# Kernel optimization log

Measured on AMD Instinct MI355X. Metric: run time of the kernel, lower is better.

Reference implementation:

```python
import jax, jax.numpy as jnp
import numpy as np


def _shift_lr(t):
    # t: [B, L, H] -> (left, right) neighbor states with zero padding
    B, L, H = t.shape
    pad = jnp.zeros((B, 1, H), dtype=t.dtype)
    left = jnp.concatenate([pad, t[:, :-1, :]], axis=1)
    right = jnp.concatenate([t[:, 1:, :], pad], axis=1)
    return left, right


def setup_inputs() -> dict:
    key = jax.random.key(0)
    ks = jax.random.split(key, 7)
    B, L, H = 32, 2048, 256
    h_t = jax.random.normal(ks[0], (B, L, H), dtype=jnp.float32)
    x = jax.random.normal(ks[1], (B, L, H), dtype=jnp.float32)
    h_slot = jax.random.normal(ks[2], (B, L, H), dtype=jnp.float32)
    h_intent = jax.random.normal(ks[3], (B, L, H), dtype=jnp.float32)
    c_t = jax.random.normal(ks[4], (B, L, H), dtype=jnp.float32)
    # gate order: [i, o, f, l, r, u]; linear in = 6H, out = H
    Ws = jax.random.normal(ks[5], (6, 6 * H, H), dtype=jnp.float32) * 0.02
    bs = jnp.zeros((6, H), dtype=jnp.float32)
    return {"h_t": h_t, "x": x, "h_slot": h_slot, "h_intent": h_intent,
            "c_t": c_t, "Ws": Ws, "bs": bs}


def reference(h_t, x, h_slot, h_intent, c_t, Ws, bs):
    h_left, h_right = _shift_lr(h_t)
    # concat order: [h_mid, h_left, h_right, x, h_slot, h_intent] -> [B,L,6H]
    cat = jnp.concatenate([h_t, h_left, h_right, x, h_slot, h_intent], axis=-1)
    # one batched GEMM for all six gates: [6, B, L, H]
    gates = jnp.einsum('blc,gch->gblh', cat, Ws) + bs[:, None, None, :]
    i_t = jax.nn.sigmoid(gates[0])
    o_t = jax.nn.sigmoid(gates[1])
    f_t = jax.nn.sigmoid(gates[2])
    l_t = jax.nn.sigmoid(gates[3])
    r_t = jax.nn.sigmoid(gates[4])
    u_t = jnp.tanh(gates[5])
    # softmax across the 4 gates (axis 0 of the stack)
    soft = jax.nn.softmax(jnp.stack([i_t, f_t, l_t, r_t], axis=0), axis=0)
    i_t, f_t, l_t, r_t = soft[0], soft[1], soft[2], soft[3]
    c_left, c_right = _shift_lr(c_t)
    c_new = f_t * c_t + l_t * c_left + r_t * c_right + i_t * u_t
    h_new = o_t * jnp.tanh(c_new)
    return (h_new, c_new)
```

## Files before the change

### kernel.cpp

```cpp
#include <hip/hip_runtime.h>

typedef __attribute__((ext_vector_type(8))) short short8;
typedef __attribute__((ext_vector_type(4))) float f32x4;

#define BB 32
#define LL 2048
#define HH 256
#define MTOT (BB*LL)
#define KK 1536
#define HSIZE (MTOT*HH)

#define SWZ4(v) (((v) & 3) ^ (((v) >> 2) & 3))

__device__ __forceinline__ unsigned short f2bf(float f){
    unsigned u = __builtin_bit_cast(unsigned, f);
    u += 0x7FFFu + ((u >> 16) & 1u);
    return (unsigned short)(u >> 16);
}
__device__ __forceinline__ unsigned pk2(float lo, float hi){
    return (unsigned)f2bf(lo) | ((unsigned)f2bf(hi) << 16);
}
__device__ __forceinline__ float sigm(float v){
    return 1.0f / (1.0f + __expf(-v));
}
__device__ __forceinline__ float ftanh(float v){
    v = fminf(fmaxf(v, -30.0f), 30.0f);
    float e = __expf(2.0f * v);
    return (e - 1.0f) / (e + 1.0f);
}
__device__ __forceinline__ void gload_lds16(const void* g, void* l){
    __builtin_amdgcn_global_load_lds(
        (const __attribute__((address_space(1))) unsigned int*)g,
        (__attribute__((address_space(3))) unsigned int*)l, 16, 0, 0);
}

__global__ __launch_bounds__(256) void prep_bt(const float* __restrict__ Ws,
                                               unsigned short* __restrict__ Bt){
    __shared__ float tile[64][65];
    int bid = blockIdx.x;
    int kb = bid % 24; int tmp = bid / 24; int hb = tmp & 3; int g = tmp >> 2;
    int t = threadIdx.x;
    const float* src = Ws + (size_t)g * (KK * HH) + (size_t)(kb * 64) * HH + hb * 64;
    #pragma unroll
    for (int it = 0; it < 16; ++it){
        int e = it * 256 + t; int kk = e >> 6, hh = e & 63;
        tile[kk][hh] = src[(size_t)kk * HH + hh];
    }
    __syncthreads();
    #pragma unroll
    for (int it = 0; it < 2; ++it){
        int jj  = t;
        int ksl = it;
        int hc  = jj >> 2, qp = jj & 3;
        int col = g * 64 + hc;
        int q   = qp ^ SWZ4(col);
        int kbase = ksl * 32 + q * 8;
        unsigned wz[4];
        #pragma unroll
        for (int p = 0; p < 4; ++p)
            wz[p] = pk2(tile[kbase + 2*p][hc], tile[kbase + 2*p + 1][hc]);
        int ksg = kb * 2 + ksl;
        size_t off = ((size_t)(hb * 48 + ksg) * 1536 + (size_t)g * 256 + jj) * 8;
        *(uint4*)&Bt[off] = *(uint4*)wz;
    }
}

__global__ __launch_bounds__(512, 2) void slstm_fused(
    const float* __restrict__ h_t, const float* __restrict__ x,
    const float* __restrict__ h_slot, const float* __restrict__ h_intent,
    const float* __restrict__ c_t, const float* __restrict__ bs,
    const unsigned short* __restrict__ Bt, float* __restrict__ out)
{
    __shared__ __align__(16) unsigned short As[2][128 * 32];
    __shared__ __align__(16) unsigned short Bs[2][384 * 32];

    const int t    = threadIdx.x;
    const int wv   = t >> 6,  ln  = t & 63;
    const int rg   = wv >> 2, ht  = wv & 3;
    const int quad = ln >> 4, l16 = ln & 15;

    const int rawb = blockIdx.x;
    const int vb   = (rawb & 7) * 256 + (rawb >> 3);
    const int h_chunk = vb & 3;
    const int m_block = vb >> 2;
    const int h0      = h_chunk * 64;

    const int  arow = t >> 2;
    const int  aq   = t & 3;
    const int  akq  = aq << 3;
    const long mg   = (long)m_block * 128 + arow;
    const int  lseq = (int)(mg & (LL - 1));
    const int  awq  = (aq ^ SWZ4(arow)) << 3;
    const int  qa   = (quad ^ SWZ4(l16)) << 3;

    const unsigned short* BtH = Bt + (size_t)h_chunk * 48 * 1536 * 8;

    f32x4 acc[4][6] = {};

    float4 av0, av1;
    auto stageA_issue = [&](int ks){
        int c  = ks >> 3;
        int kk = ((ks & 7) << 5) + akq;
        const float* src; int sh;
        switch (c){
            case 0:  src = h_t;      sh =  0; break;
            case 1:  src = h_t;      sh = -1; break;
            case 2:  src = h_t;      sh =  1; break;
            case 3:  src = x;        sh =  0; break;
            case 4:  src = h_slot;   sh =  0; break;
            default: src = h_intent; sh =  0; break;
        }
        int sl = lseq + sh;
        av0 = make_float4(0.f,0.f,0.f,0.f); av1 = av0;
        if ((unsigned)sl < (unsigned)LL){
            const float* p = src + ((mg + sh) * HH + kk);
            av0 = *(const float4*)p;
            av1 = *(const float4*)(p + 4);
        }
    };
    auto stageB = [&](int buf, int ks){
        const unsigned short* gsrc = BtH + (size_t)ks * 1536 * 8;
        #pragma unroll
        for (int i = 0; i < 3; ++i){
            gload_lds16(gsrc + (size_t)(i * 512 + t) * 8,
                        &Bs[buf][(i * 512 + wv * 64) * 8]);
        }
    };
    auto stageA_write = [&](int buf){
        uint4 w;
        w.x = pk2(av0.x, av0.y); w.y = pk2(av0.z, av0.w);
        w.z = pk2(av1.x, av1.y); w.w = pk2(av1.z, av1.w);
        *(uint4*)&As[buf][arow * 32 + awq] = w;
    };

    stageA_issue(0);
    stageB(0, 0);
    stageA_write(0);
    __syncthreads();

    for (int ks = 0; ks < 48; ++ks){
        const int cur = ks & 1, nxt = cur ^ 1;
        if (ks < 47){
            stageA_issue(ks + 1);
            stageB(nxt, ks + 1);
        }
        short8 a[4];
        #pragma unroll
        for (int mt = 0; mt < 4; ++mt)
            a[mt] = *(const short8*)&As[cur][(rg * 64 + mt * 16 + l16) * 32 + qa];
        #pragma unroll
        for (int g = 0; g < 6; ++g){
            short8 bfrag = *(const short8*)&Bs[cur][(g * 64 + ht * 16 + l16) * 32 + qa];
            #pragma unroll
            for (int mt = 0; mt < 4; ++mt)
                acc[mt][g] = __builtin_amdgcn_mfma_f32_16x16x32_bf16(a[mt], bfrag, acc[mt][g], 0, 0, 0);
        }
        if (ks < 47) stageA_write(nxt);
        __syncthreads();
    }

    const int h = h0 + ht * 16 + l16;
    float bias[6];
    #pragma unroll
    for (int g = 0; g < 6; ++g) bias[g] = bs[g * HH + h];

    #pragma unroll
    for (int mt = 0; mt < 4; ++mt){
        #pragma unroll
        for (int r = 0; r < 4; ++r){
            long row = (long)m_block * 128 + rg * 64 + mt * 16 + quad * 4 + r;
            int  ls  = (int)(row & (LL - 1));
            float gi = sigm(acc[mt][0][r] + bias[0]);
            float go = sigm(acc[mt][1][r] + bias[1]);
            float gf = sigm(acc[mt][2][r] + bias[2]);
            float gl = sigm(acc[mt][3][r] + bias[3]);
            float gr = sigm(acc[mt][4][r] + bias[4]);
            float gu = ftanh(acc[mt][5][r] + bias[5]);
            float ei = __expf(gi), ef = __expf(gf), el = __expf(gl), er = __expf(gr);
            float inv = 1.0f / (ei + ef + el + er);
            float cm  = c_t[row * HH + h];
            float clv = (ls > 0)      ? c_t[(row - 1) * HH + h] : 0.0f;
            float crv = (ls < LL - 1) ? c_t[(row + 1) * HH + h] : 0.0f;
            float cn  = (ef * cm + el * clv + er * crv + ei * gu) * inv;
            float hn  = go * ftanh(cn);
            out[row * HH + h]         = hn;
            out[HSIZE + row * HH + h] = cn;
        }
    }
}

extern "C" void kernel_launch(void* const* d_in, const int* in_sizes, int n_in,
                              void* d_out, int out_size, void* d_ws, size_t ws_size,
                              hipStream_t stream){
    const float* h_t      = (const float*)d_in[0];
    const float* x        = (const float*)d_in[1];
    const float* h_slot   = (const float*)d_in[2];
    const float* h_intent = (const float*)d_in[3];
    const float* c_t      = (const float*)d_in[4];
    const float* Ws       = (const float*)d_in[5];
    const float* bs       = (const float*)d_in[6];
    unsigned short* Bt    = (unsigned short*)d_ws;

    prep_bt<<<576, 256, 0, stream>>>(Ws, Bt);
    slstm_fused<<<2048, 512, 0, stream>>>(h_t, x, h_slot, h_intent, c_t, bs, Bt, (float*)d_out);
}
```

Measured before the change: 826.5 us.

## Pre-convert activations to bf16 and stage A tiles via direct global-to-LDS loads

```diff
diff --git a/kernel.cpp b/kernel.cpp
--- a/kernel.cpp
+++ b/kernel.cpp
@@ -65,11 +65,31 @@
     }
 }
 
-__global__ __launch_bounds__(512, 2) void slstm_fused(
+__global__ __launch_bounds__(256) void prep_a16(
     const float* __restrict__ h_t, const float* __restrict__ x,
     const float* __restrict__ h_slot, const float* __restrict__ h_intent,
-    const float* __restrict__ c_t, const float* __restrict__ bs,
-    const unsigned short* __restrict__ Bt, float* __restrict__ out)
+    unsigned short* __restrict__ A16)
+{
+    const size_t nslots = (size_t)4 * HSIZE / 8;
+    for (size_t s = (size_t)blockIdx.x * 256 + threadIdx.x; s < nslots;
+         s += (size_t)gridDim.x * 256){
+        size_t tsr = s >> 21;
+        size_t w   = s & ((1u << 21) - 1);
+        const float* src = (tsr == 0) ? h_t : (tsr == 1) ? x
+                         : (tsr == 2) ? h_slot : h_intent;
+        const float4 v0 = *(const float4*)(src + w * 8);
+        const float4 v1 = *(const float4*)(src + w * 8 + 4);
+        uint4 o;
+        o.x = pk2(v0.x, v0.y); o.y = pk2(v0.z, v0.w);
+        o.z = pk2(v1.x, v1.y); o.w = pk2(v1.z, v1.w);
+        *(uint4*)(A16 + s * 8) = o;
+    }
+}
+
+__global__ __launch_bounds__(512, 2) void slstm_fused2(
+    const unsigned short* __restrict__ A16, const float* __restrict__ c_t,
+    const float* __restrict__ bs, const unsigned short* __restrict__ Bt,
+    float* __restrict__ out)
 {
     __shared__ __align__(16) unsigned short As[2][128 * 32];
     __shared__ __align__(16) unsigned short Bs[2][384 * 32];
@@ -87,36 +107,29 @@
 
     const int  arow = t >> 2;
     const int  aq   = t & 3;
-    const int  akq  = aq << 3;
+    const int  asq  = (aq ^ SWZ4(arow)) << 3;
     const long mg   = (long)m_block * 128 + arow;
-    const int  lseq = (int)(mg & (LL - 1));
-    const int  awq  = (aq ^ SWZ4(arow)) << 3;
     const int  qa   = (quad ^ SWZ4(l16)) << 3;
 
     const unsigned short* BtH = Bt + (size_t)h_chunk * 48 * 1536 * 8;
 
     f32x4 acc[4][6] = {};
 
-    float4 av0, av1;
-    auto stageA_issue = [&](int ks){
-        int c  = ks >> 3;
-        int kk = ((ks & 7) << 5) + akq;
-        const float* src; int sh;
+    auto stageA = [&](int buf, int ks){
+        int c = ks >> 3; int tsel, sh;
         switch (c){
-            case 0:  src = h_t;      sh =  0; break;
-            case 1:  src = h_t;      sh = -1; break;
-            case 2:  src = h_t;      sh =  1; break;
-            case 3:  src = x;        sh =  0; break;
-            case 4:  src = h_slot;   sh =  0; break;
-            default: src = h_intent; sh =  0; break;
-        }
-        int sl = lseq + sh;
-        av0 = make_float4(0.f,0.f,0.f,0.f); av1 = av0;
-        if ((unsigned)sl < (unsigned)LL){
-            const float* p = src + ((mg + sh) * HH + kk);
-            av0 = *(const float4*)p;
-            av1 = *(const float4*)(p + 4);
-        }
+            case 0:  tsel = 0; sh =  0; break;
+            case 1:  tsel = 0; sh = -1; break;
+            case 2:  tsel = 0; sh =  1; break;
+            case 3:  tsel = 1; sh =  0; break;
+            case 4:  tsel = 2; sh =  0; break;
+            default: tsel = 3; sh =  0; break;
+        }
+        long srow = mg + sh;
+        srow = srow < 0 ? 0 : (srow > (long)MTOT - 1 ? (long)MTOT - 1 : srow);
+        const unsigned short* src =
+            A16 + (size_t)tsel * HSIZE + (size_t)srow * HH + ((ks & 7) << 5) + asq;
+        gload_lds16(src, &As[buf][wv * 16 * 32]);
     };
     auto stageB = [&](int buf, int ks){
         const unsigned short* gsrc = BtH + (size_t)ks * 1536 * 8;
@@ -126,24 +139,33 @@
                         &Bs[buf][(i * 512 + wv * 64) * 8]);
         }
     };
-    auto stageA_write = [&](int buf){
-        uint4 w;
-        w.x = pk2(av0.x, av0.y); w.y = pk2(av0.z, av0.w);
-        w.z = pk2(av1.x, av1.y); w.w = pk2(av1.z, av1.w);
-        *(uint4*)&As[buf][arow * 32 + awq] = w;
-    };
-
-    stageA_issue(0);
+
+    stageA(0, 0);
     stageB(0, 0);
-    stageA_write(0);
     __syncthreads();
+
+    const bool mb_first = (m_block & 15) == 0;
+    const bool mb_last  = (m_block & 15) == 15;
 
     for (int ks = 0; ks < 48; ++ks){
         const int cur = ks & 1, nxt = cur ^ 1;
+
+        {
+            int c = ks >> 3;
+            bool fix0   = (c == 1) && mb_first;
+            bool fix127 = (c == 2) && mb_last;
+            if (fix0 || fix127){
+                int br = fix0 ? 0 : 127;
+                if (t < 4) *(uint4*)&As[cur][br * 32 + t * 8] = make_uint4(0,0,0,0);
+                __syncthreads();
+            }
+        }
+
         if (ks < 47){
-            stageA_issue(ks + 1);
+            stageA(nxt, ks + 1);
             stageB(nxt, ks + 1);
         }
+
         short8 a[4];
         #pragma unroll
         for (int mt = 0; mt < 4; ++mt)
@@ -155,7 +177,6 @@
             for (int mt = 0; mt < 4; ++mt)
                 acc[mt][g] = __builtin_amdgcn_mfma_f32_16x16x32_bf16(a[mt], bfrag, acc[mt][g], 0, 0, 0);
         }
-        if (ks < 47) stageA_write(nxt);
         __syncthreads();
     }
 
@@ -189,6 +210,130 @@
     }
 }
 
+__global__ __launch_bounds__(512, 2) void slstm_fused(
+    const float* __restrict__ h_t, const float* __restrict__ x,
+    const float* __restrict__ h_slot, const float* __restrict__ h_intent,
+    const float* __restrict__ c_t, const float* __restrict__ bs,
+    const unsigned short* __restrict__ Bt, float* __restrict__ out)
+{
+    __shared__ __align__(16) unsigned short As[2][128 * 32];
+    __shared__ __align__(16) unsigned short Bs[2][384 * 32];
+
+    const int t    = threadIdx.x;
+    const int wv   = t >> 6,  ln  = t & 63;
+    const int rg   = wv >> 2, ht  = wv & 3;
+    const int quad = ln >> 4, l16 = ln & 15;
+
+    const int rawb = blockIdx.x;
+    const int vb   = (rawb & 7) * 256 + (rawb >> 3);
+    const int h_chunk = vb & 3;
+    const int m_block = vb >> 2;
+    const int h0      = h_chunk * 64;
+
+    const int  arow = t >> 2;
+    const int  aq   = t & 3;
+    const int  akq  = aq << 3;
+    const long mg   = (long)m_block * 128 + arow;
+    const int  lseq = (int)(mg & (LL - 1));
+    const int  awq  = (aq ^ SWZ4(arow)) << 3;
+    const int  qa   = (quad ^ SWZ4(l16)) << 3;
+
+    const unsigned short* BtH = Bt + (size_t)h_chunk * 48 * 1536 * 8;
+
+    f32x4 acc[4][6] = {};
+
+    float4 av0, av1;
+    auto stageA_issue = [&](int ks){
+        int c  = ks >> 3;
+        int kk = ((ks & 7) << 5) + akq;
+        const float* src; int sh;
+        switch (c){
+            case 0:  src = h_t;      sh =  0; break;
+            case 1:  src = h_t;      sh = -1; break;
+            case 2:  src = h_t;      sh =  1; break;
+            case 3:  src = x;        sh =  0; break;
+            case 4:  src = h_slot;   sh =  0; break;
+            default: src = h_intent; sh =  0; break;
+        }
+        int sl = lseq + sh;
+        av0 = make_float4(0.f,0.f,0.f,0.f); av1 = av0;
+        if ((unsigned)sl < (unsigned)LL){
+            const float* p = src + ((mg + sh) * HH + kk);
+            av0 = *(const float4*)p;
+            av1 = *(const float4*)(p + 4);
+        }
+    };
+    auto stageB = [&](int buf, int ks){
+        const unsigned short* gsrc = BtH + (size_t)ks * 1536 * 8;
+        #pragma unroll
+        for (int i = 0; i < 3; ++i){
+            gload_lds16(gsrc + (size_t)(i * 512 + t) * 8,
+                        &Bs[buf][(i * 512 + wv * 64) * 8]);
+        }
+    };
+    auto stageA_write = [&](int buf){
+        uint4 w;
+        w.x = pk2(av0.x, av0.y); w.y = pk2(av0.z, av0.w);
+        w.z = pk2(av1.x, av1.y); w.w = pk2(av1.z, av1.w);
+        *(uint4*)&As[buf][arow * 32 + awq] = w;
+    };
+
+    stageA_issue(0);
+    stageB(0, 0);
+    stageA_write(0);
+    __syncthreads();
+
+    for (int ks = 0; ks < 48; ++ks){
+        const int cur = ks & 1, nxt = cur ^ 1;
+        if (ks < 47){
+            stageA_issue(ks + 1);
+            stageB(nxt, ks + 1);
+        }
+        short8 a[4];
+        #pragma unroll
+        for (int mt = 0; mt < 4; ++mt)
+            a[mt] = *(const short8*)&As[cur][(rg * 64 + mt * 16 + l16) * 32 + qa];
+        #pragma unroll
+        for (int g = 0; g < 6; ++g){
+            short8 bfrag = *(const short8*)&Bs[cur][(g * 64 + ht * 16 + l16) * 32 + qa];
+            #pragma unroll
+            for (int mt = 0; mt < 4; ++mt)
+                acc[mt][g] = __builtin_amdgcn_mfma_f32_16x16x32_bf16(a[mt], bfrag, acc[mt][g], 0, 0, 0);
+        }
+        if (ks < 47) stageA_write(nxt);
+        __syncthreads();
+    }
+
+    const int h = h0 + ht * 16 + l16;
+    float bias[6];
+    #pragma unroll
+    for (int g = 0; g < 6; ++g) bias[g] = bs[g * HH + h];
+
+    #pragma unroll
+    for (int mt = 0; mt < 4; ++mt){
+        #pragma unroll
+        for (int r = 0; r < 4; ++r){
+            long row = (long)m_block * 128 + rg * 64 + mt * 16 + quad * 4 + r;
+            int  ls  = (int)(row & (LL - 1));
+            float gi = sigm(acc[mt][0][r] + bias[0]);
+            float go = sigm(acc[mt][1][r] + bias[1]);
+            float gf = sigm(acc[mt][2][r] + bias[2]);
+            float gl = sigm(acc[mt][3][r] + bias[3]);
+            float gr = sigm(acc[mt][4][r] + bias[4]);
+            float gu = ftanh(acc[mt][5][r] + bias[5]);
+            float ei = __expf(gi), ef = __expf(gf), el = __expf(gl), er = __expf(gr);
+            float inv = 1.0f / (ei + ef + el + er);
+            float cm  = c_t[row * HH + h];
+            float clv = (ls > 0)      ? c_t[(row - 1) * HH + h] : 0.0f;
+            float crv = (ls < LL - 1) ? c_t[(row + 1) * HH + h] : 0.0f;
+            float cn  = (ef * cm + el * clv + er * crv + ei * gu) * inv;
+            float hn  = go * ftanh(cn);
+            out[row * HH + h]         = hn;
+            out[HSIZE + row * HH + h] = cn;
+        }
+    }
+}
+
 extern "C" void kernel_launch(void* const* d_in, const int* in_sizes, int n_in,
                               void* d_out, int out_size, void* d_ws, size_t ws_size,
                               hipStream_t stream){
@@ -199,8 +344,18 @@
     const float* c_t      = (const float*)d_in[4];
     const float* Ws       = (const float*)d_in[5];
     const float* bs       = (const float*)d_in[6];
-    unsigned short* Bt    = (unsigned short*)d_ws;
+
+    unsigned short* Bt = (unsigned short*)d_ws;
+    const size_t bt_elems = (size_t)KK * KK;
+    const size_t need = bt_elems * 2 + (size_t)4 * HSIZE * 2;
 
     prep_bt<<<576, 256, 0, stream>>>(Ws, Bt);
-    slstm_fused<<<2048, 512, 0, stream>>>(h_t, x, h_slot, h_intent, c_t, bs, Bt, (float*)d_out);
-}
+
+    if (ws_size >= need){
+        unsigned short* A16 = Bt + bt_elems;
+        prep_a16<<<4096, 256, 0, stream>>>(h_t, x, h_slot, h_intent, A16);
+        slstm_fused2<<<2048, 512, 0, stream>>>(A16, c_t, bs, Bt, (float*)d_out);
+    } else {
+        slstm_fused<<<2048, 512, 0, stream>>>(h_t, x, h_slot, h_intent, c_t, bs, Bt, (float*)d_out);
+    }
+}
```

Result: slower. 866.2 us (+4.8%).
